# Performance work log

Measured on AMD Instinct MI355X. Metric: run time of the kernel, lower is better.

The kernel has to match this reference:

```python
import jax, jax.numpy as jnp
import numpy as np

NVEC = (3, 3, 4, 25, 25, 8)  # MultiDiscrete sub-action sizes; sum = 68


def _segmented_log_softmax(x, axis=-1):
    """log_softmax applied independently within each sub-action segment along last dim."""
    parts = []
    s = 0
    for n in NVEC:
        parts.append(jax.nn.log_softmax(x[..., s:s + n], axis=axis))
        s += n
    return jnp.concatenate(parts, axis=-1)


def setup_inputs() -> dict:
    key = jax.random.key(0)
    k1, k2 = jax.random.split(key)
    A = int(sum(NVEC))
    W = 524288
    current_action = jax.random.normal(k1, (A,), dtype=jnp.float32)
    previous_actions = jax.random.normal(k2, (W, A), dtype=jnp.float32)
    return {"current_action": current_action, "previous_actions": previous_actions}


def reference(current_action, previous_actions):
    W = previous_actions.shape[0]
    # logits=True path: segmented log_softmax on both inputs
    x = _segmented_log_softmax(current_action)          # [A] log-probs (KLDiv 'input')
    t = _segmented_log_softmax(previous_actions)        # [W, A] log-probs (KLDiv 'target', log_target=True)
    # KLDivLoss(log_target=True): exp(t) * (t - x); reduction='batchmean' on a 1D
    # slice of length n_j divides by n_j (input.size(0)).
    inv_n = jnp.asarray(np.repeat(1.0 / np.asarray(NVEC, dtype=np.float32), NVEC))  # [A]
    loss = jnp.sum(jnp.exp(t) * (t - x[None, :]) * inv_n[None, :])
    return loss / W
```

## Files before the change

kernel.cpp:

```cpp
#include <hip/hip_runtime.h>


namespace {
constexpr int kA = 68;
constexpr int kNSeg = 6;
constexpr int kOff[kNSeg + 1] = {0, 3, 6, 10, 35, 60, 68};
constexpr float kInvN[kNSeg] = {1.f/3.f, 1.f/3.f, 1.f/4.f, 1.f/25.f, 1.f/25.f, 1.f/8.f};
}

__global__ __launch_bounds__(256) void asl_kernel(
    const float* __restrict__ cur,
    const float* __restrict__ prev,
    float* __restrict__ out,
    int W, float invW)
{
    __shared__ float xs[kA];
    __shared__ float wsum[4];

    const int tid = threadIdx.x;

    if (tid < kNSeg) {
        const int o = kOff[tid], e = kOff[tid + 1];
        float m = cur[o];
        for (int j = o + 1; j < e; ++j) m = fmaxf(m, cur[j]);
        float s = 0.f;
        for (int j = o; j < e; ++j) s += __expf(cur[j] - m);
        const float L = m + __logf(s);
        for (int j = o; j < e; ++j) xs[j] = cur[j] - L;
    }
    __syncthreads();

    const int row = blockIdx.x * blockDim.x + tid;
    float acc = 0.f;
    if (row < W) {
        float v[kA];
        const float4* rp = (const float4*)(prev + (size_t)row * kA);
        #pragma unroll
        for (int k = 0; k < kA / 4; ++k) ((float4*)v)[k] = rp[k];

        #pragma unroll
        for (int sg = 0; sg < kNSeg; ++sg) {
            const int o = kOff[sg];
            const int n = kOff[sg + 1] - kOff[sg];
            float m = v[o];
            #pragma unroll
            for (int j = 1; j < n; ++j) m = fmaxf(m, v[o + j]);
            float s = 0.f, d = 0.f;
            #pragma unroll
            for (int j = 0; j < n; ++j) {
                const float e = __expf(v[o + j] - m);
                s += e;
                d += e * (v[o + j] - xs[o + j]);
            }
            const float L = m + __logf(s);
            acc += kInvN[sg] * (d / s - L);
        }
        acc *= invW;
    }

    #pragma unroll
    for (int o2 = 32; o2 > 0; o2 >>= 1) acc += __shfl_down(acc, o2, 64);
    const int wave = tid >> 6;
    if ((tid & 63) == 0) wsum[wave] = acc;
    __syncthreads();
    if (tid == 0) {
        atomicAdd(out, wsum[0] + wsum[1] + wsum[2] + wsum[3]);
    }
}

extern "C" void kernel_launch(void* const* d_in, const int* in_sizes, int n_in,
                              void* d_out, int out_size, void* d_ws, size_t ws_size,
                              hipStream_t stream) {
    const float* cur  = (const float*)d_in[0];
    const float* prev = (const float*)d_in[1];
    float* out = (float*)d_out;

    const int W = in_sizes[1] / kA;

    hipMemsetAsync(out, 0, sizeof(float), stream);

    const int block = 256;
    const int grid = (W + block - 1) / block;
    asl_kernel<<<grid, block, 0, stream>>>(cur, prev, out, W, 1.0f / (float)W);
}
```

Before: 221.9 us.

## Stage row tiles through LDS with double-buffered async loads in persistent grid

Replaces the one-row-per-thread strided global reads with a persistent 512-block grid. Each block streams 128-row tiles into double-buffered LDS using coalesced global_load_lds with an XOR swizzle, then splits each row's segments across two threads. It also drops the max-subtraction in the log-softmax and uses a reciprocal instead of a divide, which removes arithmetic but can overflow if logits are large. The aim is to turn the uncoalesced per-thread 272-byte row loads into bandwidth-friendly streaming and to overlap loading with compute.

```diff
diff --git a/kernel.cpp b/kernel.cpp
--- a/kernel.cpp
+++ b/kernel.cpp
@@ -3,69 +3,123 @@
 
 namespace {
 constexpr int kA = 68;
+constexpr int kF4 = 17;
 constexpr int kNSeg = 6;
 constexpr int kOff[kNSeg + 1] = {0, 3, 6, 10, 35, 60, 68};
 constexpr float kInvN[kNSeg] = {1.f/3.f, 1.f/3.f, 1.f/4.f, 1.f/25.f, 1.f/25.f, 1.f/8.f};
+constexpr int kTileRows = 128;
+constexpr int kTileF4 = kTileRows * kF4;
+constexpr int kChunks = kTileF4 / 64;
+constexpr int kGrid = 512;
 }
 
 __global__ __launch_bounds__(256) void asl_kernel(
     const float* __restrict__ cur,
     const float* __restrict__ prev,
     float* __restrict__ out,
-    int W, float invW)
+    int W, int numTiles, float invW)
 {
+    __shared__ float4 buf[2][kTileF4];
     __shared__ float xs[kA];
     __shared__ float wsum[4];
 
-    const int tid = threadIdx.x;
+    const int tid  = threadIdx.x;
+    const int wave = tid >> 6;
+    const int lane = tid & 63;
+    const int swzl = lane ^ ((lane >> 3) & 7);
 
     if (tid < kNSeg) {
         const int o = kOff[tid], e = kOff[tid + 1];
-        float m = cur[o];
-        for (int j = o + 1; j < e; ++j) m = fmaxf(m, cur[j]);
         float s = 0.f;
-        for (int j = o; j < e; ++j) s += __expf(cur[j] - m);
-        const float L = m + __logf(s);
+        for (int j = o; j < e; ++j) s += __expf(cur[j]);
+        const float L = __logf(s);
         for (int j = o; j < e; ++j) xs[j] = cur[j] - L;
     }
-    __syncthreads();
 
-    const int row = blockIdx.x * blockDim.x + tid;
+    const float4* prev4 = (const float4*)prev;
+    const long totalF4 = (long)W * kF4;
+
+    auto stage = [&](int b, int t) {
+        const long base = (long)t * kTileF4;
+        #pragma unroll
+        for (int k = 0; k < 9; ++k) {
+            const int ch = wave + 4 * k;
+            if (ch >= kChunks) break;
+            long g = base + ch * 64 + swzl;
+            if (g >= totalF4) g = totalF4 - 1;
+            __builtin_amdgcn_global_load_lds(
+                (const __attribute__((address_space(1))) void*)(prev4 + g),
+                (__attribute__((address_space(3))) void*)(&buf[b][ch * 64]),
+                16, 0, 0);
+        }
+    };
+
+    const int half = tid >> 7;
+    const int r    = tid & 127;
+    const int c0   = half * 8;
     float acc = 0.f;
-    if (row < W) {
-        float v[kA];
-        const float4* rp = (const float4*)(prev + (size_t)row * kA);
-        #pragma unroll
-        for (int k = 0; k < kA / 4; ++k) ((float4*)v)[k] = rp[k];
+    int buf_i = 0;
+    int tile  = blockIdx.x;
+    if (tile < numTiles) stage(0, tile);
 
-        #pragma unroll
-        for (int sg = 0; sg < kNSeg; ++sg) {
-            const int o = kOff[sg];
-            const int n = kOff[sg + 1] - kOff[sg];
-            float m = v[o];
+    for (; tile < numTiles; tile += kGrid) {
+        __syncthreads();
+        const int nt = tile + kGrid;
+        if (nt < numTiles) stage(buf_i ^ 1, nt);
+
+        float vloc[36];
+        {
+            const float4* bp = buf[buf_i];
+            const int qb = r * kF4 + c0;
             #pragma unroll
-            for (int j = 1; j < n; ++j) m = fmaxf(m, v[o + j]);
-            float s = 0.f, d = 0.f;
-            #pragma unroll
-            for (int j = 0; j < n; ++j) {
-                const float e = __expf(v[o + j] - m);
-                s += e;
-                d += e * (v[o + j] - xs[o + j]);
+            for (int k = 0; k < 9; ++k) {
+                const int q  = qb + k;
+                const int qs = q ^ ((q >> 3) & 7);
+                ((float4*)vloc)[k] = bp[qs];
             }
-            const float L = m + __logf(s);
-            acc += kInvN[sg] * (d / s - L);
         }
-        acc *= invW;
+
+        const int rowg = tile * kTileRows + r;
+        if (rowg < W) {
+            if (half == 0) {
+                #pragma unroll
+                for (int sg = 0; sg < 4; ++sg) {
+                    const int o = kOff[sg], n = kOff[sg + 1] - kOff[sg];
+                    float s = 0.f, d = 0.f;
+                    #pragma unroll
+                    for (int j = 0; j < n; ++j) {
+                        const float x = vloc[o + j];
+                        const float e = __expf(x);
+                        s += e;
+                        d = fmaf(e, x - xs[o + j], d);
+                    }
+                    acc += kInvN[sg] * (d * __builtin_amdgcn_rcpf(s) - __logf(s));
+                }
+            } else {
+                #pragma unroll
+                for (int sg = 4; sg < 6; ++sg) {
+                    const int o = kOff[sg], n = kOff[sg + 1] - kOff[sg];
+                    float s = 0.f, d = 0.f;
+                    #pragma unroll
+                    for (int j = 0; j < n; ++j) {
+                        const float x = vloc[o - 32 + j];
+                        const float e = __expf(x);
+                        s += e;
+                        d = fmaf(e, x - xs[o + j], d);
+                    }
+                    acc += kInvN[sg] * (d * __builtin_amdgcn_rcpf(s) - __logf(s));
+                }
+            }
+        }
+        buf_i ^= 1;
     }
 
+    acc *= invW;
     #pragma unroll
     for (int o2 = 32; o2 > 0; o2 >>= 1) acc += __shfl_down(acc, o2, 64);
-    const int wave = tid >> 6;
-    if ((tid & 63) == 0) wsum[wave] = acc;
+    if (lane == 0) wsum[wave] = acc;
     __syncthreads();
-    if (tid == 0) {
-        atomicAdd(out, wsum[0] + wsum[1] + wsum[2] + wsum[3]);
-    }
+    if (tid == 0) atomicAdd(out, wsum[0] + wsum[1] + wsum[2] + wsum[3]);
 }
 
 extern "C" void kernel_launch(void* const* d_in, const int* in_sizes, int n_in,
@@ -76,10 +130,8 @@
     float* out = (float*)d_out;
 
     const int W = in_sizes[1] / kA;
+    const int numTiles = (W + kTileRows - 1) / kTileRows;
 
     hipMemsetAsync(out, 0, sizeof(float), stream);
-
-    const int block = 256;
-    const int grid = (W + block - 1) / block;
-    asl_kernel<<<grid, block, 0, stream>>>(cur, prev, out, W, 1.0f / (float)W);
+    asl_kernel<<<kGrid, 256, 0, stream>>>(cur, prev, out, W, numTiles, 1.0f / (float)W);
 }
```

Result: faster. 205.2 us (-7.5%).

## Coalesce row loads via per-wave LDS transpose with persistent double-buffered tiles

Applied to the files above, without the earlier changes.

Each wave loads a 64-row tile as contiguous float4 chunks, so global loads are fully coalesced, then transposes the tile through XOR-swizzled LDS so each lane reads back its own row. A persistent grid of 512 blocks walks tiles with register double buffering, so the next tile's loads overlap the current tile's math. The max-subtraction in log-softmax is dropped and the division is replaced by a hardware reciprocal. These changes cut instruction count, but they can overflow for large logits and reduce precision. The larger LDS footprint and register double buffering also raise per-thread resource use.

```diff
diff --git a/kernel.cpp b/kernel.cpp
--- a/kernel.cpp
+++ b/kernel.cpp
@@ -3,69 +3,112 @@
 
 namespace {
 constexpr int kA = 68;
+constexpr int kF4 = 17;
 constexpr int kNSeg = 6;
 constexpr int kOff[kNSeg + 1] = {0, 3, 6, 10, 35, 60, 68};
 constexpr float kInvN[kNSeg] = {1.f/3.f, 1.f/3.f, 1.f/4.f, 1.f/25.f, 1.f/25.f, 1.f/8.f};
+constexpr int kRows = 64;
+constexpr int kTileF4 = kRows * kF4;
+constexpr int kGrid = 512;
+constexpr int kWPB = 4;
 }
 
 __global__ __launch_bounds__(256) void asl_kernel(
     const float* __restrict__ cur,
     const float* __restrict__ prev,
     float* __restrict__ out,
-    int W, float invW)
+    int W, int numTiles, float invW)
 {
+    __shared__ float4 buf[kWPB][kTileF4];
     __shared__ float xs[kA];
-    __shared__ float wsum[4];
+    __shared__ float wsum[kWPB];
 
-    const int tid = threadIdx.x;
+    const int tid  = threadIdx.x;
+    const int wave = tid >> 6;
+    const int lane = tid & 63;
 
     if (tid < kNSeg) {
         const int o = kOff[tid], e = kOff[tid + 1];
-        float m = cur[o];
-        for (int j = o + 1; j < e; ++j) m = fmaxf(m, cur[j]);
         float s = 0.f;
-        for (int j = o; j < e; ++j) s += __expf(cur[j] - m);
-        const float L = m + __logf(s);
+        for (int j = o; j < e; ++j) s += __expf(cur[j]);
+        const float L = __logf(s);
         for (int j = o; j < e; ++j) xs[j] = cur[j] - L;
     }
     __syncthreads();
 
-    const int row = blockIdx.x * blockDim.x + tid;
+    const float4* prev4 = (const float4*)prev;
+    const long totalF4 = (long)W * kF4;
+    float4* wbuf = buf[wave];
+
+    auto loadT = [&](float4 (&r)[kF4], long t) {
+        const long base = t * (long)kTileF4 + lane;
+        #pragma unroll
+        for (int c = 0; c < kF4; ++c) {
+            long g = base + 64 * c;
+            if (g >= totalF4) g = totalF4 - 1;
+            r[c] = prev4[g];
+        }
+    };
+
+    auto consume = [&](float4 (&r)[kF4], long t, float& acc) {
+        #pragma unroll
+        for (int c = 0; c < kF4; ++c) {
+            const int q = 64 * c + lane;
+            wbuf[q ^ ((q >> 3) & 7)] = r[c];
+        }
+        if (t * (long)kRows + lane < W) {
+            float v[kA];
+            const int qb = lane * kF4;
+            #pragma unroll
+            for (int c = 0; c < kF4; ++c) {
+                const int q = qb + c;
+                ((float4*)v)[c] = wbuf[q ^ ((q >> 3) & 7)];
+            }
+            float racc = 0.f;
+            #pragma unroll
+            for (int sg = 0; sg < kNSeg; ++sg) {
+                const int o = kOff[sg], n = kOff[sg + 1] - kOff[sg];
+                float s = 0.f, d = 0.f;
+                #pragma unroll
+                for (int j = 0; j < n; ++j) {
+                    const float x = v[o + j];
+                    const float e = __expf(x);
+                    s += e;
+                    d = fmaf(e, x - xs[o + j], d);
+                }
+                racc += kInvN[sg] * (d * __builtin_amdgcn_rcpf(s) - __logf(s));
+            }
+            acc += racc;
+        }
+    };
+
+    const long stride = (long)kGrid * kWPB;
+    long t = (long)blockIdx.x * kWPB + wave;
     float acc = 0.f;
-    if (row < W) {
-        float v[kA];
-        const float4* rp = (const float4*)(prev + (size_t)row * kA);
-        #pragma unroll
-        for (int k = 0; k < kA / 4; ++k) ((float4*)v)[k] = rp[k];
 
-        #pragma unroll
-        for (int sg = 0; sg < kNSeg; ++sg) {
-            const int o = kOff[sg];
-            const int n = kOff[sg + 1] - kOff[sg];
-            float m = v[o];
-            #pragma unroll
-            for (int j = 1; j < n; ++j) m = fmaxf(m, v[o + j]);
-            float s = 0.f, d = 0.f;
-            #pragma unroll
-            for (int j = 0; j < n; ++j) {
-                const float e = __expf(v[o + j] - m);
-                s += e;
-                d += e * (v[o + j] - xs[o + j]);
-            }
-            const float L = m + __logf(s);
-            acc += kInvN[sg] * (d / s - L);
-        }
-        acc *= invW;
+    float4 rA[kF4], rB[kF4];
+    bool haveA = (t < numTiles);
+    if (haveA) loadT(rA, t);
+    while (haveA) {
+        const long tB = t + stride;
+        const bool haveB = (tB < numTiles);
+        if (haveB) loadT(rB, tB);
+        consume(rA, t, acc);
+        if (!haveB) break;
+        const long tA2 = tB + stride;
+        const bool haveA2 = (tA2 < numTiles);
+        if (haveA2) loadT(rA, tA2);
+        consume(rB, tB, acc);
+        t = tA2;
+        haveA = haveA2;
     }
 
+    acc *= invW;
     #pragma unroll
     for (int o2 = 32; o2 > 0; o2 >>= 1) acc += __shfl_down(acc, o2, 64);
-    const int wave = tid >> 6;
-    if ((tid & 63) == 0) wsum[wave] = acc;
+    if (lane == 0) wsum[wave] = acc;
     __syncthreads();
-    if (tid == 0) {
-        atomicAdd(out, wsum[0] + wsum[1] + wsum[2] + wsum[3]);
-    }
+    if (tid == 0) atomicAdd(out, wsum[0] + wsum[1] + wsum[2] + wsum[3]);
 }
 
 extern "C" void kernel_launch(void* const* d_in, const int* in_sizes, int n_in,
@@ -76,10 +119,8 @@
     float* out = (float*)d_out;
 
     const int W = in_sizes[1] / kA;
+    const int numTiles = (W + kRows - 1) / kRows;
 
     hipMemsetAsync(out, 0, sizeof(float), stream);
-
-    const int block = 256;
-    const int grid = (W + block - 1) / block;
-    asl_kernel<<<grid, block, 0, stream>>>(cur, prev, out, W, 1.0f / (float)W);
+    asl_kernel<<<kGrid, 256, 0, stream>>>(cur, prev, out, W, numTiles, 1.0f / (float)W);
 }
```

New measurement: 237.5 us. 7.0% more time.
